# Performance work log

Hardware: AMD Instinct MI355X
Metric: run time of the kernel (lower is better)

The kernel has to match this reference:

```python
import jax, jax.numpy as jnp
import numpy as np

HD = 1960            # 40 channels * 49 kernel taps
KH = KW = 7
PH = PW = 3
SH = SW = 3


def _patch_idx(out_len, k, s):
    return (jnp.arange(out_len) * s)[:, None] + jnp.arange(k)[None, :]  # [out_len, k]


def _unfold(img, kh, kw, ph, pw, sh, sw):
    # img: [N, C, Hi, Wi] -> cols: [N, C*kh*kw, Hout*Wout]  (torch F.unfold layout)
    N, C, Hi, Wi = img.shape
    Hout = (Hi + 2 * ph - kh) // sh + 1
    Wout = (Wi + 2 * pw - kw) // sw + 1
    xp = jnp.pad(img, ((0, 0), (0, 0), (ph, ph), (pw, pw)))
    ii = _patch_idx(Hout, kh, sh)  # [Hout, kh]
    jj = _patch_idx(Wout, kw, sw)  # [Wout, kw]
    p = xp[:, :, ii[:, :, None, None], jj[None, None, :, :]]  # [N,C,Hout,kh,Wout,kw]
    p = p.transpose(0, 1, 3, 5, 2, 4).reshape(N, C * kh * kw, Hout * Wout)
    return p


def _fold(cols, out_h, out_w, kh, kw, ph, pw, sh, sw):
    # cols: [N, C*kh*kw, L] -> img: [N, C, out_h, out_w]  (torch F.fold overlap-add)
    N, CK, L = cols.shape
    C = CK // (kh * kw)
    Hout = (out_h + 2 * ph - kh) // sh + 1
    Wout = (out_w + 2 * pw - kw) // sw + 1
    p = cols.reshape(N, C, kh, kw, Hout, Wout).transpose(0, 1, 4, 2, 5, 3)  # [N,C,Hout,kh,Wout,kw]
    ii = _patch_idx(Hout, kh, sh)
    jj = _patch_idx(Wout, kw, sw)
    out = jnp.zeros((N, C, out_h + 2 * ph, out_w + 2 * pw), cols.dtype)
    out = out.at[:, :, ii[:, :, None, None], jj[None, None, :, :]].add(p)
    return out[:, :, ph:out_h + ph, pw:out_w + pw]


def _dwconv(x, w, b, pad):
    # depthwise conv, x: [N,C,H,W], w: [C,1,k,k]
    y = jax.lax.conv_general_dilated(
        x, w, window_strides=(1, 1), padding=[(pad, pad), (pad, pad)],
        dimension_numbers=('NCHW', 'OIHW', 'NCHW'), feature_group_count=x.shape[1])
    return y + b[None, :, None, None]


def setup_inputs() -> dict:
    key = jax.random.key(0)
    ks = jax.random.split(key, 6)
    d_model = 512
    x = jax.random.normal(ks[0], (2, 5760, d_model), dtype=jnp.float32)
    w1 = jax.random.normal(ks[1], (d_model, HD), dtype=jnp.float32) * 0.02
    b1 = jnp.zeros((HD,), jnp.float32)
    w3 = jax.random.normal(ks[2], (HD // 2, 1, 3, 3), dtype=jnp.float32) * 0.1
    b3 = jnp.zeros((HD // 2,), jnp.float32)
    w5 = jax.random.normal(ks[3], (HD - HD // 2, 1, 5, 5), dtype=jnp.float32) * 0.05
    b5 = jnp.zeros((HD - HD // 2,), jnp.float32)
    w2 = jax.random.normal(ks[4], (HD, d_model), dtype=jnp.float32) * 0.02
    b2 = jnp.zeros((d_model,), jnp.float32)
    return dict(x=x, w1=w1, b1=b1, w3=w3, b3=b3, w5=w5, b5=b5, w2=w2, b2=b2,
                out_h=60, out_w=108, T=8, H=20, W=36)


def reference(x, w1, b1, w3, b3, w5, b5, w2, b2, out_h, out_w, T, H, W):
    n_vecs = ((out_h + 2 * PH - KH) // SH + 1) * ((out_w + 2 * PW - KW) // SW + 1)
    x = x @ w1 + b1                                   # [b, n, hd]
    b, n, c = x.shape
    cols = x.reshape(-1, n_vecs, c).transpose(0, 2, 1)  # [b*T, hd, n_vecs]
    bt = cols.shape[0]
    img = _fold(cols, out_h, out_w, KH, KW, PH, PW, SH, SW)           # [b*T, 40, out_h, out_w]
    norm = _fold(jnp.ones((bt, KH * KW, n_vecs), x.dtype),
                 out_h, out_w, KH, KW, PH, PW, SH, SW)                # [b*T, 1, out_h, out_w]
    cols2 = _unfold(img / norm, KH, KW, PH, PW, SH, SW)               # [b*T, hd, n_vecs]
    x = cols2.transpose(0, 2, 1).reshape(b, n, c)
    x = x.reshape(b * T, H, W, c).transpose(0, 3, 1, 2)               # [b*T, hd, H, W]
    h = c // 2
    y = jnp.concatenate([_dwconv(x[:, :h], w3, b3, 1),
                         _dwconv(x[:, h:], w5, b5, 2)], axis=1)       # MixConv2d (depthwise 3x3 / 5x5)
    y = y.transpose(0, 2, 3, 1).reshape(b, n, c)
    return jax.nn.gelu(y, approximate=False) @ w2 + b2
```

## Files before the change

kernel.cpp:

```cpp
#include <hip/hip_runtime.h>
#include <cstdint>

typedef short v8s __attribute__((ext_vector_type(8)));
typedef float v4f __attribute__((ext_vector_type(4)));
typedef unsigned short u16;

#define M_ROWS 11520
#define K1 512
#define N1 2048
#define C_REAL 1960
#define K2 1984
#define N2 512
#define TPAD 56
#define PLANE_ELEMS (720 * TPAD)
#define HROW 2016

__device__ __forceinline__ u16 f2b(float f) {
  union { float f; unsigned u; } v; v.f = f;
  unsigned r = v.u + 0x7FFFu + ((v.u >> 16) & 1u);
  return (u16)(r >> 16);
}
__device__ __forceinline__ float b2f(u16 b) {
  union { unsigned u; float f; } v; v.u = ((unsigned)b) << 16; return v.f;
}

__device__ __forceinline__ void gl2lds16(const u16* g, u16* l) {
  __builtin_amdgcn_global_load_lds(
      (const __attribute__((address_space(1))) unsigned int*)g,
      (__attribute__((address_space(3))) unsigned int*)l, 16, 0, 0);
}

__global__ void cast_x8(const float* __restrict__ x, u16* __restrict__ xb) {
  int i = blockIdx.x * 256 + threadIdx.x;
  const float4 a = ((const float4*)x)[2 * i];
  const float4 b = ((const float4*)x)[2 * i + 1];
  u16 o[8] = {f2b(a.x), f2b(a.y), f2b(a.z), f2b(a.w),
              f2b(b.x), f2b(b.y), f2b(b.z), f2b(b.w)};
  ((int4*)xb)[i] = *(const int4*)o;
}

__global__ __launch_bounds__(256) void transpose_cast(
    const float* __restrict__ src, u16* __restrict__ dst, int R, int C, int KP)
{
  __shared__ float T[32][33];
  const int n0 = blockIdx.x * 32, k0 = blockIdx.y * 32;
  const int tx = threadIdx.x & 31, ty = threadIdx.x >> 5;
  #pragma unroll
  for (int r = 0; r < 4; ++r) {
    int k = k0 + ty + 8 * r, n = n0 + tx;
    T[ty + 8 * r][tx] = (k < R && n < C) ? src[(size_t)k * C + n] : 0.f;
  }
  __syncthreads();
  #pragma unroll
  for (int r = 0; r < 4; ++r) {
    int n = n0 + ty + 8 * r, k = k0 + tx;
    if (k < KP) dst[(size_t)n * KP + k] = f2b(T[tx][ty + 8 * r]);
  }
}

__global__ void zero_gpad(u16* __restrict__ G) {
  int i = blockIdx.x * 256 + threadIdx.x;
  int r = i / 24, j = i - r * 24;
  G[(size_t)r * K2 + C_REAL + j] = 0;
}

__device__ __forceinline__ void stv(float v, float* p) { *p = v; }
__device__ __forceinline__ void stv(float v, u16* p) { *p = f2b(v); }

template<typename OT, bool FOLD>
__global__ __launch_bounds__(256) void gemm_bt(
    const u16* __restrict__ A, const u16* __restrict__ BT,
    const float* __restrict__ bias, int nb, OT* __restrict__ C, int N, int K)
{
  __shared__ u16 As[128 * 64];
  __shared__ u16 Bs[128 * 64];
  const int tid = threadIdx.x;
  const int bm = blockIdx.y * 128, bn = blockIdx.x * 128;
  const int wave = tid >> 6, lane = tid & 63;
  const int quad = lane >> 4, l16 = lane & 15;
  const int wm = (wave >> 1) * 64, wn = (wave & 1) * 64;
  const int srow = lane >> 3;
  const int scol = ((lane & 7) ^ srow) * 8;

  const u16* pA = A + (size_t)(bm + wave * 32 + srow) * K + scol;
  const u16* pB = BT + (size_t)(bn + wave * 32 + srow) * K + scol;
  u16* lA = As + (wave * 32) * 64;
  u16* lB = Bs + (wave * 32) * 64;

  v4f acc[4][4];
  #pragma unroll
  for (int i = 0; i < 4; ++i)
    #pragma unroll
    for (int j = 0; j < 4; ++j) acc[i][j] = (v4f){0.f, 0.f, 0.f, 0.f};

  for (int k0 = 0; k0 < K; k0 += 64) {
    #pragma unroll
    for (int q = 0; q < 4; ++q) {
      gl2lds16(pA + (size_t)(q * 8) * K, lA + q * 8 * 64);
      gl2lds16(pB + (size_t)(q * 8) * K, lB + q * 8 * 64);
    }
    pA += 64; pB += 64;
    __syncthreads();
    #pragma unroll
    for (int h = 0; h < 2; ++h) {
      v8s af[4], bf[4];
      #pragma unroll
      for (int i = 0; i < 4; ++i) {
        int row = wm + i * 16 + l16;
        int ck = (h * 4 + quad) ^ (row & 7);
        af[i] = *(const v8s*)&As[row * 64 + ck * 8];
      }
      #pragma unroll
      for (int j = 0; j < 4; ++j) {
        int row = wn + j * 16 + l16;
        int ck = (h * 4 + quad) ^ (row & 7);
        bf[j] = *(const v8s*)&Bs[row * 64 + ck * 8];
      }
      #pragma unroll
      for (int i = 0; i < 4; ++i)
        #pragma unroll
        for (int j = 0; j < 4; ++j)
          acc[i][j] = __builtin_amdgcn_mfma_f32_16x16x32_bf16(af[i], bf[j], acc[i][j], 0, 0, 0);
    }
    __syncthreads();
  }

  #pragma unroll
  for (int i = 0; i < 4; ++i) {
    #pragma unroll
    for (int j = 0; j < 4; ++j) {
      int col = bn + wn + j * 16 + l16;
      if (FOLD && col >= C_REAL) continue;
      float bv = (col < nb) ? bias[col] : 0.f;
      int ch = 0, t = 0;
      if (FOLD) { ch = col / 49; t = col - ch * 49; }
      #pragma unroll
      for (int r = 0; r < 4; ++r) {
        int row = bm + wm + i * 16 + quad * 4 + r;
        float val = acc[i][j][r] + bv;
        if (FOLD) {
          int bt = row / 720, v = row - bt * 720;
          stv(val, C + (size_t)(bt * 40 + ch) * PLANE_ELEMS + v * TPAD + t);
        } else {
          stv(val, C + (size_t)row * N + col);
        }
      }
    }
  }
}

__global__ __launch_bounds__(256) void fold_norm(const u16* __restrict__ Aw,
                                                 float* __restrict__ Sn)
{
  __shared__ u16 raw[10 * HROW];
  const int plane = blockIdx.y;
  const int r0 = blockIdx.x * 22;
  const int tid = threadIdx.x;
  const int hlo = max(0, (r0 - 6) / 3);
  const int hhi = min(19, (r0 + 21) / 3);
  const int nchunks = (hhi - hlo + 1) * (HROW / 8);
  const int4* src = (const int4*)(Aw + (size_t)plane * PLANE_ELEMS + hlo * HROW);
  int4* dst = (int4*)raw;
  for (int j = tid; j < nchunks; j += 256) dst[j] = src[j];
  __syncthreads();

  float* out = Sn + (size_t)plane * 7524 + r0 * 114;
  for (int i = tid; i < 22 * 114; i += 256) {
    int r = i / 114, px = i - r * 114;
    int py = r0 + r;
    float val = 0.f;
    if (py >= 3 && py < 63 && px >= 3 && px < 111) {
      int ry = py % 3, rx = px % 3;
      int hhs[3], kis[3], nki = 0;
      #pragma unroll
      for (int k = 0; k < 3; ++k) {
        int ki = ry + 3 * k;
        if (ki < 7 && py - ki >= 0) {
          int hh = (py - ki) / 3;
          if (hh < 20) { kis[nki] = ki; hhs[nki] = hh; ++nki; }
        }
      }
      int wws[3], kjs[3], nkj = 0;
      #pragma unroll
      for (int k = 0; k < 3; ++k) {
        int kj = rx + 3 * k;
        if (kj < 7 && px - kj >= 0) {
          int ww = (px - kj) / 3;
          if (ww < 36) { kjs[nkj] = kj; wws[nkj] = ww; ++nkj; }
        }
      }
      float sum = 0.f;
      for (int a = 0; a < nki; ++a) {
        int rowoff = (hhs[a] - hlo) * HROW + kis[a] * 7;
        for (int b = 0; b < nkj; ++b)
          sum += b2f(raw[rowoff + wws[b] * TPAD + kjs[b]]);
      }
      val = sum / (float)(nki * nkj);
    }
    out[i] = val;
  }
}

template<int KS>
__device__ __forceinline__ void conv_part(const float* __restrict__ Sl,
    const float* __restrict__ Wl, const float* __restrict__ Bl,
    u16* __restrict__ G, int bt, int colbase, int h0, int tid)
{
  constexpr int P = KS / 2;
  const int rbase = 3 * h0 - 6;
  for (int idx = tid; idx < 36 * 49; idx += 256) {
    int wo = idx / 49, t = idx - wo * 49;
    int ki = t / 7, kj = t - ki * 7;
    float wgt[KS * KS];
    #pragma unroll
    for (int j = 0; j < KS * KS; ++j) wgt[j] = Wl[t * KS * KS + j];
    const float bias = Bl[t];
    int sx[KS]; bool vx[KS];
    #pragma unroll
    for (int dx = 0; dx < KS; ++dx) {
      int wq = wo + dx - P;
      vx[dx] = (wq >= 0 && wq < 36);
      sx[dx] = wq * 3 + kj;
    }
    float win[KS][KS];
    #pragma unroll
    for (int dy = 0; dy < KS; ++dy) {
      int hq = h0 + dy - P;
      #pragma unroll
      for (int dx = 0; dx < KS; ++dx)
        win[dy][dx] = (hq >= 0 && hq < 20 && vx[dx])
                        ? Sl[(hq * 3 + ki - rbase) * 114 + sx[dx]] : 0.f;
    }
    u16* gp = G + (size_t)(bt * 720 + h0 * 36 + wo) * K2 + colbase + t;
    #pragma unroll
    for (int hh = 0; hh < 4; ++hh) {
      float y = bias;
      #pragma unroll
      for (int dy = 0; dy < KS; ++dy)
        #pragma unroll
        for (int dx = 0; dx < KS; ++dx)
          y += wgt[dy * KS + dx] * win[dy][dx];
      float g = 0.5f * y * (1.0f + erff(y * 0.70710678118654752f));
      *gp = f2b(g);
      gp += (size_t)36 * K2;
      if (hh < 3) {
        #pragma unroll
        for (int dy = 0; dy < KS - 1; ++dy)
          #pragma unroll
          for (int dx = 0; dx < KS; ++dx) win[dy][dx] = win[dy + 1][dx];
        int hq = h0 + hh + 1 + P;
        #pragma unroll
        for (int dx = 0; dx < KS; ++dx)
          win[KS - 1][dx] = (hq < 20 && vx[dx])
                              ? Sl[(hq * 3 + ki - rbase) * 114 + sx[dx]] : 0.f;
      }
    }
  }
}

__global__ __launch_bounds__(256) void dwconv_gelu2(const float* __restrict__ Sn,
    const float* __restrict__ w3, const float* __restrict__ b3,
    const float* __restrict__ w5, const float* __restrict__ b5,
    u16* __restrict__ G)
{
  __shared__ float Sl[28 * 114];
  __shared__ float Wl[49 * 25];
  __shared__ float Bl[49];
  const int plane = blockIdx.y, bt = plane / 40, ch = plane % 40;
  const int h0 = blockIdx.x * 4;
  const int tid = threadIdx.x;
  const int colbase = ch * 49;
  const bool is3 = (ch < 20);
  if (is3) {
    for (int i = tid; i < 49 * 9; i += 256) Wl[i] = w3[colbase * 9 + i];
    if (tid < 49) Bl[tid] = b3[colbase + tid];
  } else {
    int c5 = colbase - 980;
    for (int i = tid; i < 49 * 25; i += 256) Wl[i] = w5[c5 * 25 + i];
    if (tid < 49) Bl[tid] = b5[c5 + tid];
  }
  const int rbase = 3 * h0 - 6;
  const float* sp = Sn + (size_t)plane * 7524;
  for (int i = tid; i < 28 * 114; i += 256) {
    int r = i / 114, c = i - r * 114;
    int py = rbase + r;
    Sl[i] = (py >= 0 && py < 66) ? sp[py * 114 + c] : 0.f;
  }
  __syncthreads();
  if (is3) conv_part<3>(Sl, Wl, Bl, G, bt, colbase, h0, tid);
  else     conv_part<5>(Sl, Wl, Bl, G, bt, colbase, h0, tid);
}

extern "C" void kernel_launch(void* const* d_in, const int* in_sizes, int n_in,
                              void* d_out, int out_size, void* d_ws, size_t ws_size,
                              hipStream_t stream) {
  const float* x  = (const float*)d_in[0];
  const float* w1 = (const float*)d_in[1];
  const float* b1 = (const float*)d_in[2];
  const float* w3 = (const float*)d_in[3];
  const float* b3 = (const float*)d_in[4];
  const float* w5 = (const float*)d_in[5];
  const float* b5 = (const float*)d_in[6];
  const float* w2 = (const float*)d_in[7];
  const float* b2 = (const float*)d_in[8];
  float* out = (float*)d_out;

  char* ws = (char*)d_ws;
  u16*   Xb  = (u16*)(ws);
  u16*   W1T = (u16*)(ws + 11796480);
  u16*   W2T = (u16*)(ws + 13893632);
  u16*   Aw  = (u16*)(ws + 15925248);
  u16*   G   = (u16*)(ws + 67534848);
  float* Sn  = (float*)(ws + 113246208);

  hipLaunchKernelGGL(cast_x8, dim3(2880), dim3(256), 0, stream, x, Xb);
  hipLaunchKernelGGL(transpose_cast, dim3(64, 16), dim3(256), 0, stream, w1, W1T, K1, C_REAL, K1);
  hipLaunchKernelGGL(transpose_cast, dim3(16, 62), dim3(256), 0, stream, w2, W2T, C_REAL, N2, K2);
  hipLaunchKernelGGL(zero_gpad, dim3(1080), dim3(256), 0, stream, G);
  hipLaunchKernelGGL((gemm_bt<u16, true>), dim3(N1 / 128, M_ROWS / 128), dim3(256), 0, stream,
                     Xb, W1T, b1, C_REAL, Aw, N1, K1);
  hipLaunchKernelGGL(fold_norm, dim3(3, 640), dim3(256), 0, stream, Aw, Sn);
  hipLaunchKernelGGL(dwconv_gelu2, dim3(5, 640), dim3(256), 0, stream,
                     Sn, w3, b3, w5, b5, G);
  hipLaunchKernelGGL((gemm_bt<float, false>), dim3(N2 / 128, M_ROWS / 128), dim3(256), 0, stream,
                     G, W2T, b2, N2, out, N2, K2);
}
```

Baseline: 286.8 us.

## Use 128x64-tile GEMM for output projection, pad conv LDS rows, fast erf GELU

Replaces the second GEMM launch with a new 128x64-tile kernel, doubling the block count (8x90 instead of 4x90) to fill more compute units on the narrow N=512 output. It also pads the dwconv shared-memory row stride from 114 to 115 floats to reduce LDS bank conflicts. The libm erff call in GELU is replaced by an Abramowitz-Stegun polynomial using hardware rcp/exp2, which is cheaper but only approximate (around 1e-7 error, below bf16 precision). The smaller tile gives less reuse per loaded element.

```diff
diff --git a/kernel.cpp b/kernel.cpp
--- a/kernel.cpp
+++ b/kernel.cpp
@@ -14,6 +14,7 @@
 #define TPAD 56
 #define PLANE_ELEMS (720 * TPAD)
 #define HROW 2016
+#define SLP 115
 
 __device__ __forceinline__ u16 f2b(float f) {
   union { float f; unsigned u; } v; v.f = f;
@@ -22,6 +23,17 @@
 }
 __device__ __forceinline__ float b2f(u16 b) {
   union { unsigned u; float f; } v; v.u = ((unsigned)b) << 16; return v.f;
+}
+
+__device__ __forceinline__ float gelu_f(float y) {
+  float z = fabsf(y) * 0.70710678118654752f;
+  float t = __builtin_amdgcn_rcpf(fmaf(0.3275911f, z, 1.0f));
+  float p = t * fmaf(t, fmaf(t, fmaf(t, fmaf(t, 1.061405429f, -1.453152027f),
+                                     1.421413741f), -0.284496736f), 0.254829592f);
+  float e = __builtin_amdgcn_exp2f(-z * z * 1.4426950408889634f);
+  float erfz = fmaf(-p, e, 1.0f);
+  float cdf = 0.5f * (1.0f + (y < 0.0f ? -erfz : erfz));
+  return y * cdf;
 }
 
 __device__ __forceinline__ void gl2lds16(const u16* g, u16* l) {
@@ -144,6 +156,79 @@
         } else {
           stv(val, C + (size_t)row * N + col);
         }
+      }
+    }
+  }
+}
+
+__global__ __launch_bounds__(256) void gemm_bt64(
+    const u16* __restrict__ A, const u16* __restrict__ BT,
+    const float* __restrict__ bias, float* __restrict__ C, int N, int K)
+{
+  __shared__ u16 As[128 * 64];
+  __shared__ u16 Bs[64 * 64];
+  const int tid = threadIdx.x;
+  const int bm = blockIdx.y * 128, bn = blockIdx.x * 64;
+  const int wave = tid >> 6, lane = tid & 63;
+  const int quad = lane >> 4, l16 = lane & 15;
+  const int wm = (wave >> 1) * 64, wn = (wave & 1) * 32;
+  const int srow = lane >> 3;
+  const int scol = ((lane & 7) ^ srow) * 8;
+
+  const u16* pA = A + (size_t)(bm + wave * 32 + srow) * K + scol;
+  const u16* pB = BT + (size_t)(bn + wave * 16 + srow) * K + scol;
+  u16* lA = As + (wave * 32) * 64;
+  u16* lB = Bs + (wave * 16) * 64;
+
+  v4f acc[4][2];
+  #pragma unroll
+  for (int i = 0; i < 4; ++i)
+    #pragma unroll
+    for (int j = 0; j < 2; ++j) acc[i][j] = (v4f){0.f, 0.f, 0.f, 0.f};
+
+  for (int k0 = 0; k0 < K; k0 += 64) {
+    #pragma unroll
+    for (int q = 0; q < 4; ++q)
+      gl2lds16(pA + (size_t)(q * 8) * K, lA + q * 8 * 64);
+    #pragma unroll
+    for (int q = 0; q < 2; ++q)
+      gl2lds16(pB + (size_t)(q * 8) * K, lB + q * 8 * 64);
+    pA += 64; pB += 64;
+    __syncthreads();
+    #pragma unroll
+    for (int h = 0; h < 2; ++h) {
+      v8s af[4], bf[2];
+      #pragma unroll
+      for (int i = 0; i < 4; ++i) {
+        int row = wm + i * 16 + l16;
+        int ck = (h * 4 + quad) ^ (row & 7);
+        af[i] = *(const v8s*)&As[row * 64 + ck * 8];
+      }
+      #pragma unroll
+      for (int j = 0; j < 2; ++j) {
+        int row = wn + j * 16 + l16;
+        int ck = (h * 4 + quad) ^ (row & 7);
+        bf[j] = *(const v8s*)&Bs[row * 64 + ck * 8];
+      }
+      #pragma unroll
+      for (int i = 0; i < 4; ++i)
+        #pragma unroll
+        for (int j = 0; j < 2; ++j)
+          acc[i][j] = __builtin_amdgcn_mfma_f32_16x16x32_bf16(af[i], bf[j], acc[i][j], 0, 0, 0);
+    }
+    __syncthreads();
+  }
+
+  #pragma unroll
+  for (int i = 0; i < 4; ++i) {
+    #pragma unroll
+    for (int j = 0; j < 2; ++j) {
+      int col = bn + wn + j * 16 + l16;
+      float bv = bias[col];
+      #pragma unroll
+      for (int r = 0; r < 4; ++r) {
+        int row = bm + wm + i * 16 + quad * 4 + r;
+        C[(size_t)row * N + col] = acc[i][j][r] + bv;
       }
     }
   }
@@ -229,7 +314,7 @@
       #pragma unroll
       for (int dx = 0; dx < KS; ++dx)
         win[dy][dx] = (hq >= 0 && hq < 20 && vx[dx])
-                        ? Sl[(hq * 3 + ki - rbase) * 114 + sx[dx]] : 0.f;
+                        ? Sl[(hq * 3 + ki - rbase) * SLP + sx[dx]] : 0.f;
     }
     u16* gp = G + (size_t)(bt * 720 + h0 * 36 + wo) * K2 + colbase + t;
     #pragma unroll
@@ -240,8 +325,7 @@
         #pragma unroll
         for (int dx = 0; dx < KS; ++dx)
           y += wgt[dy * KS + dx] * win[dy][dx];
-      float g = 0.5f * y * (1.0f + erff(y * 0.70710678118654752f));
-      *gp = f2b(g);
+      *gp = f2b(gelu_f(y));
       gp += (size_t)36 * K2;
       if (hh < 3) {
         #pragma unroll
@@ -252,7 +336,7 @@
         #pragma unroll
         for (int dx = 0; dx < KS; ++dx)
           win[KS - 1][dx] = (hq < 20 && vx[dx])
-                              ? Sl[(hq * 3 + ki - rbase) * 114 + sx[dx]] : 0.f;
+                              ? Sl[(hq * 3 + ki - rbase) * SLP + sx[dx]] : 0.f;
       }
     }
   }
@@ -263,7 +347,7 @@
     const float* __restrict__ w5, const float* __restrict__ b5,
     u16* __restrict__ G)
 {
-  __shared__ float Sl[28 * 114];
+  __shared__ float Sl[28 * SLP];
   __shared__ float Wl[49 * 25];
   __shared__ float Bl[49];
   const int plane = blockIdx.y, bt = plane / 40, ch = plane % 40;
@@ -284,7 +368,7 @@
   for (int i = tid; i < 28 * 114; i += 256) {
     int r = i / 114, c = i - r * 114;
     int py = rbase + r;
-    Sl[i] = (py >= 0 && py < 66) ? sp[py * 114 + c] : 0.f;
+    Sl[r * SLP + c] = (py >= 0 && py < 66) ? sp[py * 114 + c] : 0.f;
   }
   __syncthreads();
   if (is3) conv_part<3>(Sl, Wl, Bl, G, bt, colbase, h0, tid);
@@ -322,6 +406,6 @@
   hipLaunchKernelGGL(fold_norm, dim3(3, 640), dim3(256), 0, stream, Aw, Sn);
   hipLaunchKernelGGL(dwconv_gelu2, dim3(5, 640), dim3(256), 0, stream,
                      Sn, w3, b3, w5, b5, G);
-  hipLaunchKernelGGL((gemm_bt<float, false>), dim3(N2 / 128, M_ROWS / 128), dim3(256), 0, stream,
-                     G, W2T, b2, N2, out, N2, K2);
-}
+  hipLaunchKernelGGL(gemm_bt64, dim3(N2 / 64, M_ROWS / 128), dim3(256), 0, stream,
+                     G, W2T, b2, out, N2, K2);
+}
```

Result: slower. 306.2 us (+6.8%).
